# Performance work log

Measured on AMD Instinct MI355X. Metric: run time of the kernel, lower is better.

## Reference

```python
import jax, jax.numpy as jnp
import numpy as np

HEAD_NUM = 6

def setup_inputs() -> dict:
    key = jax.random.key(0)
    k1, k2, k3 = jax.random.split(key, 3)
    B, N, P, C = 4, 64, 256, 384
    x = jax.random.normal(k1, (B, N, P, C), dtype=jnp.float32)
    # torch Linear init scale ~ 1/sqrt(fan_in); keep magnitudes sane
    w_qkv = jax.random.normal(k2, (C, 3 * C), dtype=jnp.float32) * (1.0 / np.sqrt(C))
    w_proj = jax.random.normal(k3, (C, C), dtype=jnp.float32) * (1.0 / np.sqrt(C))
    b_proj = jnp.zeros((C,), dtype=jnp.float32)
    return {"x": x, "w_qkv": w_qkv, "w_proj": w_proj, "b_proj": b_proj}

def reference(x, w_qkv, w_proj, b_proj):
    B, N, P, C = x.shape
    H = HEAD_NUM
    D = C // H
    scale = jnp.asarray(D, dtype=x.dtype)  # NOTE: head_dim ** 1, faithful to source
    qkv = (x @ w_qkv).reshape(B, N, P, 3, H, D)
    q = qkv[:, :, :, 0]  # (B, N, P, H, D)
    k = qkv[:, :, :, 1]
    v = qkv[:, :, :, 2]
    attn = jnp.einsum('bnphd,bnqhd->bnhpq', q, k) * scale  # (B,N,H,P,P)
    attn = jax.nn.softmax(attn, axis=-1)
    out = jnp.einsum('bnhpq,bnqhd->bnphd', attn, v).reshape(B, N, P, C)
    return out @ w_proj + b_proj
```

## Files before the change

### kernel.cpp

```cpp
#include <hip/hip_runtime.h>

typedef __bf16 bf16_t;
typedef __bf16 bf16x8 __attribute__((ext_vector_type(8)));
typedef float f32x4 __attribute__((ext_vector_type(4)));
typedef unsigned short u16;
typedef unsigned short u16x4 __attribute__((ext_vector_type(4)));
typedef unsigned int u32;

#define B_ 4
#define N_ 64
#define P_ 256
#define C_ 384
#define H_ 6
#define D_ 64
#define M_TOTAL 65536
#define NQKV 1152
#define KSTEPS 12
#define NBLK (H_*B_*N_)
#define WKS_BYTES 24576
#define WKS_U16   12288
#define FUSED_LDS 139264
#define PB_STRIDE 40
#define SB() __builtin_amdgcn_sched_barrier(0)

#define GLOAD_LDS16(g, l) __builtin_amdgcn_global_load_lds( \
    (const __attribute__((address_space(1))) void*)(g), \
    (__attribute__((address_space(3))) void*)(l), 16, 0, 0)

__device__ __forceinline__ u16 f2b(float f){ return __builtin_bit_cast(u16, (bf16_t)f); }
__device__ __forceinline__ f32x4 mfma(bf16x8 a, bf16x8 b, f32x4 c){
    return __builtin_amdgcn_mfma_f32_16x16x32_bf16(a, b, c, 0, 0, 0);
}

__global__ __launch_bounds__(256) void prep_w(
    const float* __restrict__ wqkv, const float* __restrict__ wproj,
    u16* __restrict__ Wpk, u16* __restrict__ wPt)
{
    int i = blockIdx.x * 256 + threadIdx.x;
    const int NSLOT = H_ * KSTEPS * 12 * 64;
    if (i < NSLOT) {
        int lane = i & 63;
        int frag = i >> 6;
        int nf = frag % 12;
        int ks = (frag / 12) % KSTEPS;
        int h  = frag / (12 * KSTEPS);
        int part = nf >> 2;
        int nh   = (nf & 3) * 16 + (lane & 15);
        int col  = part * C_ + h * 64 + nh;
        int k0   = ks * 32 + (lane >> 4) * 8;
        size_t base = (size_t)(h * KSTEPS + ks) * WKS_U16 + nf * 512 + lane * 8;
        #pragma unroll
        for (int e = 0; e < 8; ++e) {
            float w = wqkv[(size_t)(k0 + e) * NQKV + col];
            bf16_t hi = (bf16_t)w;
            Wpk[base + e]        = __builtin_bit_cast(u16, hi);
            Wpk[base + 6144 + e] = f2b(w - (float)hi);
        }
    }
    int j = i - NSLOT;
    if (j >= 0 && j < C_ * C_) {
        int k = j / C_, n = j % C_;
        wPt[(size_t)n * C_ + k] = f2b(wproj[j]);
    }
}

__global__ __launch_bounds__(512, 2) void fused_attn(
    const float* __restrict__ x, const u16* __restrict__ Wpk,
    u16* __restrict__ attn)
{
    extern __shared__ u16 sm[];
    u16* Kh = sm;
    u16* Kl = sm + 16384;
    u16* Vt = sm + 32768;
    u16* Qb = sm + 49152;

    const int tid  = threadIdx.x;
    const int lane = tid & 63, wid = tid >> 6;
    const int g = lane >> 4, r16 = lane & 15;

    const int p = blockIdx.x;
    const int logical = (p & 7) * (NBLK / 8) + (p >> 3);
    const int h  = logical % H_;
    const int bn = logical / H_;
    const size_t row0 = (size_t)bn * P_;
    const int m0w = wid * 32;

    f32x4 acc[2][12];
    #pragma unroll
    for (int mf = 0; mf < 2; ++mf)
        #pragma unroll
        for (int nf = 0; nf < 12; ++nf) acc[mf][nf] = f32x4{0.f,0.f,0.f,0.f};

    const float* xr0 = x + (row0 + m0w + r16) * C_;
    const float* xr1 = xr0 + 16 * C_;
    const char* wbase = (const char*)Wpk + (size_t)h * (KSTEPS * WKS_BYTES);

#define STAGE(ks_, par_) do { \
    const char* _gp = wbase + (size_t)(ks_) * WKS_BYTES; \
    char* _lp = (char*)(sm + (par_) * WKS_U16); \
    GLOAD_LDS16(_gp + tid * 16,          _lp + tid * 16); \
    GLOAD_LDS16(_gp + 8192 + tid * 16,   _lp + 8192 + tid * 16); \
    GLOAD_LDS16(_gp + 16384 + tid * 16,  _lp + 16384 + tid * 16); \
} while (0)

    f32x4 xr[2][4];
#define XLOAD(ks_, par_) do { \
    const float* _xp0 = xr0 + (ks_) * 32 + 8 * g; \
    const float* _xp1 = xr1 + (ks_) * 32 + 8 * g; \
    xr[par_][0] = *(const f32x4*)_xp0; xr[par_][1] = *(const f32x4*)(_xp0 + 4); \
    xr[par_][2] = *(const f32x4*)_xp1; xr[par_][3] = *(const f32x4*)(_xp1 + 4); \
} while (0)

    bf16x8 ah[2], al[2];
#define SPLIT_A(par_) do { \
    _Pragma("unroll") \
    for (int e = 0; e < 4; ++e) { \
        bf16_t h0 = (bf16_t)xr[par_][0][e], h1 = (bf16_t)xr[par_][1][e]; \
        ah[0][e]   = h0; al[0][e]   = (bf16_t)(xr[par_][0][e] - (float)h0); \
        ah[0][4+e] = h1; al[0][4+e] = (bf16_t)(xr[par_][1][e] - (float)h1); \
        bf16_t h2 = (bf16_t)xr[par_][2][e], h3 = (bf16_t)xr[par_][3][e]; \
        ah[1][e]   = h2; al[1][e]   = (bf16_t)(xr[par_][2][e] - (float)h2); \
        ah[1][4+e] = h3; al[1][4+e] = (bf16_t)(xr[par_][3][e] - (float)h3); \
    } } while (0)

    STAGE(0, 0);
    XLOAD(0, 0);
    __syncthreads();

    #pragma unroll
    for (int ks = 0; ks < KSTEPS; ++ks) {
        const int par = ks & 1, nxt = par ^ 1;
        if (ks < KSTEPS - 1) {
            STAGE(ks + 1, nxt);
            XLOAD(ks + 1, nxt);
        }
        SPLIT_A(par);
        const u16* stg = sm + par * WKS_U16;
        #pragma unroll
        for (int nf = 0; nf < 8; ++nf) {
            bf16x8 bh = *(const bf16x8*)&stg[nf * 512 + lane * 8];
            bf16x8 bl = *(const bf16x8*)&stg[6144 + nf * 512 + lane * 8];
            acc[0][nf] = mfma(ah[0], bh, acc[0][nf]);
            acc[1][nf] = mfma(ah[1], bh, acc[1][nf]);
            acc[0][nf] = mfma(ah[0], bl, acc[0][nf]);
            acc[1][nf] = mfma(ah[1], bl, acc[1][nf]);
            acc[0][nf] = mfma(al[0], bh, acc[0][nf]);
            acc[1][nf] = mfma(al[1], bh, acc[1][nf]);
        }
        #pragma unroll
        for (int nf = 8; nf < 12; ++nf) {
            bf16x8 bh = *(const bf16x8*)&stg[nf * 512 + lane * 8];
            acc[0][nf] = mfma(ah[0], bh, acc[0][nf]);
            acc[1][nf] = mfma(ah[1], bh, acc[1][nf]);
        }
        __syncthreads();
    }

    #pragma unroll
    for (int mf = 0; mf < 2; ++mf)
    #pragma unroll
    for (int f = 0; f < 4; ++f)
    #pragma unroll
    for (int rr = 0; rr < 4; ++rr) {
        int q = m0w + mf * 16 + 4 * g + rr;
        int d = f * 16 + r16;
        int ek = q * 64 + (((d >> 3) ^ (q & 7)) << 3) + (d & 7);
        float kv = acc[mf][4 + f][rr];
        bf16_t khi = (bf16_t)kv;
        Kh[ek] = __builtin_bit_cast(u16, khi);
        Kl[ek] = f2b(kv - (float)khi);
        Vt[d * 256 + (((q >> 3) ^ (d & 7)) << 3) + (q & 7)] = f2b(acc[mf][8 + f][rr]);
    }

    u16* myQb = Qb + wid * 2560;
    bf16x8 aqh[2][2], aql[2][2];
    #pragma unroll
    for (int mf = 0; mf < 2; ++mf)
    #pragma unroll
    for (int f = 0; f < 4; ++f)
    #pragma unroll
    for (int rr = 0; rr < 4; ++rr) {
        int r = mf * 16 + 4 * g + rr;
        int c = f * 16 + r16;
        myQb[r * 64 + (((c >> 3) ^ (r & 7)) << 3) + (c & 7)] = f2b(acc[mf][f][rr]);
    }
    #pragma unroll
    for (int mf = 0; mf < 2; ++mf)
    #pragma unroll
    for (int k2 = 0; k2 < 2; ++k2) {
        int r = mf * 16 + r16;
        aqh[mf][k2] = *(const bf16x8*)&myQb[r * 64 + (((k2 * 4 + g) ^ (r & 7)) << 3)];
    }
    SB();
    #pragma unroll
    for (int mf = 0; mf < 2; ++mf)
    #pragma unroll
    for (int f = 0; f < 4; ++f)
    #pragma unroll
    for (int rr = 0; rr < 4; ++rr) {
        int r = mf * 16 + 4 * g + rr;
        int c = f * 16 + r16;
        float v = acc[mf][f][rr];
        bf16_t hi = (bf16_t)v;
        myQb[r * 64 + (((c >> 3) ^ (r & 7)) << 3) + (c & 7)] = f2b(v - (float)hi);
    }
    #pragma unroll
    for (int mf = 0; mf < 2; ++mf)
    #pragma unroll
    for (int k2 = 0; k2 < 2; ++k2) {
        int r = mf * 16 + r16;
        aql[mf][k2] = *(const bf16x8*)&myQb[r * 64 + (((k2 * 4 + g) ^ (r & 7)) << 3)];
    }

    __syncthreads();

    f32x4 S[2][16];
    #pragma unroll
    for (int mf = 0; mf < 2; ++mf)
        #pragma unroll
        for (int nf = 0; nf < 16; ++nf) S[mf][nf] = f32x4{0.f,0.f,0.f,0.f};

    bf16x8 khv[2][2], klv[2][2];
    {
        int q = r16;
        #pragma unroll
        for (int k2 = 0; k2 < 2; ++k2) {
            int e = q * 64 + (((k2 * 4 + g) ^ (q & 7)) << 3);
            khv[0][k2] = *(const bf16x8*)&Kh[e];
            klv[0][k2] = *(const bf16x8*)&Kl[e];
        }
    }
    #pragma unroll
    for (int nf = 0; nf < 16; ++nf) {
        const int par = nf & 1, nxt = par ^ 1;
        if (nf < 15) {
            int q = (nf + 1) * 16 + r16;
            #pragma unroll
            for (int k2 = 0; k2 < 2; ++k2) {
                int e = q * 64 + (((k2 * 4 + g) ^ (q & 7)) << 3);
                khv[nxt][k2] = *(const bf16x8*)&Kh[e];
                klv[nxt][k2] = *(const bf16x8*)&Kl[e];
            }
        }
        SB();
        __builtin_amdgcn_s_setprio(1);
        #pragma unroll
        for (int k2 = 0; k2 < 2; ++k2) {
            S[0][nf] = mfma(aqh[0][k2], khv[par][k2], S[0][nf]);
            S[1][nf] = mfma(aqh[1][k2], khv[par][k2], S[1][nf]);
            S[0][nf] = mfma(aqh[0][k2], klv[par][k2], S[0][nf]);
            S[1][nf] = mfma(aqh[1][k2], klv[par][k2], S[1][nf]);
            S[0][nf] = mfma(aql[0][k2], khv[par][k2], S[0][nf]);
            S[1][nf] = mfma(aql[1][k2], khv[par][k2], S[1][nf]);
        }
        __builtin_amdgcn_s_setprio(0);
        SB();
    }

    float inv_[2][4];
    #pragma unroll
    for (int mf = 0; mf < 2; ++mf) {
        float mrow[4] = {-1e30f,-1e30f,-1e30f,-1e30f};
        #pragma unroll
        for (int nf = 0; nf < 16; ++nf)
            #pragma unroll
            for (int rr = 0; rr < 4; ++rr) mrow[rr] = fmaxf(mrow[rr], S[mf][nf][rr]);
        #pragma unroll
        for (int mask = 1; mask < 16; mask <<= 1)
            #pragma unroll
            for (int rr = 0; rr < 4; ++rr) mrow[rr] = fmaxf(mrow[rr], __shfl_xor(mrow[rr], mask, 64));
        float ssum[4] = {0.f,0.f,0.f,0.f};
        #pragma unroll
        for (int nf = 0; nf < 16; ++nf)
            #pragma unroll
            for (int rr = 0; rr < 4; ++rr) {
                float pv = __expf((S[mf][nf][rr] - mrow[rr]) * 64.0f);
                S[mf][nf][rr] = pv;
                ssum[rr] += pv;
            }
        #pragma unroll
        for (int mask = 1; mask < 16; mask <<= 1)
            #pragma unroll
            for (int rr = 0; rr < 4; ++rr) ssum[rr] += __shfl_xor(ssum[rr], mask, 64);
        #pragma unroll
        for (int rr = 0; rr < 4; ++rr) inv_[mf][rr] = 1.0f / ssum[rr];
    }

    f32x4 O[2][4];
    #pragma unroll
    for (int mf = 0; mf < 2; ++mf)
        #pragma unroll
        for (int f = 0; f < 4; ++f) O[mf][f] = f32x4{0.f,0.f,0.f,0.f};

    bf16x8 bvv[2][4];
    #pragma unroll
    for (int f = 0; f < 4; ++f) {
        int d = f * 16 + r16;
        bvv[0][f] = *(const bf16x8*)&Vt[d * 256 + ((((8 * g) >> 3) ^ (d & 7)) << 3)];
    }
    #pragma unroll
    for (int t = 0; t < 8; ++t) {
        const int par = t & 1, nxt = par ^ 1;
        if (t < 7) {
            #pragma unroll
            for (int f = 0; f < 4; ++f) {
                int d = f * 16 + r16;
                bvv[nxt][f] = *(const bf16x8*)&Vt[d * 256 + (((((t + 1) * 32 + 8 * g) >> 3) ^ (d & 7)) << 3)];
            }
        }
        u16* pb = myQb + par * 1280;
        #pragma unroll
        for (int mf = 0; mf < 2; ++mf)
        #pragma unroll
        for (int tt = 0; tt < 2; ++tt) {
            int nf = 2 * t + tt;
            #pragma unroll
            for (int rr = 0; rr < 4; ++rr)
                pb[(mf * 16 + 4 * g + rr) * PB_STRIDE + tt * 16 + r16] = f2b(S[mf][nf][rr] * inv_[mf][rr]);
        }
        bf16x8 ap0 = *(const bf16x8*)&pb[(r16) * PB_STRIDE + 8 * g];
        bf16x8 ap1 = *(const bf16x8*)&pb[(16 + r16) * PB_STRIDE + 8 * g];
        __builtin_amdgcn_s_setprio(1);
        #pragma unroll
        for (int f = 0; f < 4; ++f) {
            O[0][f] = mfma(ap0, bvv[par][f], O[0][f]);
            O[1][f] = mfma(ap1, bvv[par][f], O[1][f]);
        }
        __builtin_amdgcn_s_setprio(0);
    }

    #pragma unroll
    for (int mf = 0; mf < 2; ++mf)
    #pragma unroll
    for (int f = 0; f < 4; ++f)
    #pragma unroll
    for (int rr = 0; rr < 4; ++rr)
        attn[(row0 + m0w + mf * 16 + 4 * g + rr) * C_ + h * 64 + f * 16 + r16] = f2b(O[mf][f][rr]);
}

__global__ __launch_bounds__(256, 2) void proj_kernel(
    const u16* __restrict__ attn, const u16* __restrict__ wPt,
    const float* __restrict__ bias, float* __restrict__ out)
{
    __shared__ alignas(16) u16 As[128*32];
    __shared__ alignas(16) u16 Bs[128*32];

    const int tid = threadIdx.x;
    const int lane = tid & 63, wid = tid >> 6;
    const int wr = wid >> 1, wc = wid & 1;
    const int g = lane >> 4, r16 = lane & 15;
    const int m0 = blockIdx.x * 128;
    const int n0 = blockIdx.y * 128;

    f32x4 acc[4][4];
    for (int i = 0; i < 4; i++) for (int j = 0; j < 4; j++) acc[i][j] = f32x4{0.f,0.f,0.f,0.f};

    for (int kt = 0; kt < C_; kt += 32) {
        for (int r = 0; r < 4; ++r) {
            int i = tid + 256*r;
            int mm = i >> 3;
            int kk = (i & 7) << 2;
            u16x4 v = *(const u16x4*)&attn[(size_t)(m0+mm)*C_ + kt + kk];
            int e = mm*32 + (((kk>>3) ^ ((mm>>1)&3))<<3) + (kk&7);
            *(u16x4*)&As[e] = v;
        }
        for (int r = 0; r < 4; ++r) {
            int i = tid + 256*r;
            int nn = i >> 3;
            int kk = (i & 7) << 2;
            u16x4 v = *(const u16x4*)&wPt[(size_t)(n0+nn)*C_ + kt + kk];
            int e = nn*32 + (((kk>>3) ^ ((nn>>1)&3))<<3) + (kk&7);
            *(u16x4*)&Bs[e] = v;
        }
        __syncthreads();

        bf16x8 a[4], b[4];
        for (int i = 0; i < 4; i++) {
            int row = wr*64 + i*16 + r16;
            a[i] = *(const bf16x8*)&As[row*32 + ((g ^ ((row>>1)&3))<<3)];
        }
        for (int j = 0; j < 4; j++) {
            int n = wc*64 + j*16 + r16;
            b[j] = *(const bf16x8*)&Bs[n*32 + ((g ^ ((n>>1)&3))<<3)];
        }
        for (int i = 0; i < 4; i++) for (int j = 0; j < 4; j++)
            acc[i][j] = mfma(a[i], b[j], acc[i][j]);
        __syncthreads();
    }

    for (int i = 0; i < 4; i++) for (int j = 0; j < 4; j++) for (int rr = 0; rr < 4; rr++) {
        size_t row = m0 + wr*64 + i*16 + g*4 + rr;
        int col = n0 + wc*64 + j*16 + r16;
        out[row*C_ + col] = acc[i][j][rr] + bias[col];
    }
}

extern "C" void kernel_launch(void* const* d_in, const int* in_sizes, int n_in,
                              void* d_out, int out_size, void* d_ws, size_t ws_size,
                              hipStream_t stream)
{
    const float* x      = (const float*)d_in[0];
    const float* w_qkv  = (const float*)d_in[1];
    const float* w_proj = (const float*)d_in[2];
    const float* b_proj = (const float*)d_in[3];
    float* out = (float*)d_out;

    u16* ws = (u16*)d_ws;
    u16* attnb = ws;
    size_t off = (size_t)M_TOTAL * C_;
    u16* Wpk = ws + off; off += (size_t)H_ * KSTEPS * WKS_U16;
    u16* wPt = ws + off; off += (size_t)C_ * C_;

    hipFuncSetAttribute((const void*)fused_attn,
                        hipFuncAttributeMaxDynamicSharedMemorySize, FUSED_LDS);

    int prep_n = H_ * KSTEPS * 12 * 64 + C_ * C_;
    prep_w<<<dim3((prep_n + 255) / 256), 256, 0, stream>>>(w_qkv, w_proj, Wpk, wPt);
    fused_attn<<<dim3(NBLK), 512, FUSED_LDS, stream>>>(x, Wpk, attnb);
    proj_kernel<<<dim3(M_TOTAL / 128, C_ / 128), 256, 0, stream>>>(attnb, wPt, b_proj, out);
}
```

Baseline: 265.6 us.

## Split fused attention across 16 waves with 16-row tiles and slimmer weight staging

The fused QKV+attention kernel goes from 512 to 1024 threads, so each wave handles 16 query rows instead of 32. This roughly halves the per-wave accumulator and score registers. The weight staging buffer drops the unused low-precision halves for the V slices, and the Q/P scratch space is moved into the freed staging region. The V-fragment double buffering is removed and softmax normalization is applied before packing P. The aim is more latency hiding from more resident waves. The risk is that the aggressive launch bound (1024, 4) forces a very tight register budget and spills, while the fixed LDS footprint still allows only one block per CU.

```diff
diff --git a/kernel.cpp b/kernel.cpp
--- a/kernel.cpp
+++ b/kernel.cpp
@@ -17,8 +17,8 @@
 #define NQKV 1152
 #define KSTEPS 12
 #define NBLK (H_*B_*N_)
-#define WKS_BYTES 24576
-#define WKS_U16   12288
+#define WKS_U16 10240
+#define WKS_BYTES 20480
 #define FUSED_LDS 139264
 #define PB_STRIDE 40
 #define SB() __builtin_amdgcn_sched_barrier(0)
@@ -48,13 +48,14 @@
         int nh   = (nf & 3) * 16 + (lane & 15);
         int col  = part * C_ + h * 64 + nh;
         int k0   = ks * 32 + (lane >> 4) * 8;
-        size_t base = (size_t)(h * KSTEPS + ks) * WKS_U16 + nf * 512 + lane * 8;
+        size_t base = (size_t)(h * KSTEPS + ks) * WKS_U16;
         #pragma unroll
         for (int e = 0; e < 8; ++e) {
             float w = wqkv[(size_t)(k0 + e) * NQKV + col];
             bf16_t hi = (bf16_t)w;
-            Wpk[base + e]        = __builtin_bit_cast(u16, hi);
-            Wpk[base + 6144 + e] = f2b(w - (float)hi);
+            Wpk[base + nf * 512 + lane * 8 + e] = __builtin_bit_cast(u16, hi);
+            if (nf < 8)
+                Wpk[base + 6144 + nf * 512 + lane * 8 + e] = f2b(w - (float)hi);
         }
     }
     int j = i - NSLOT;
@@ -64,7 +65,7 @@
     }
 }
 
-__global__ __launch_bounds__(512, 2) void fused_attn(
+__global__ __launch_bounds__(1024, 4) void fused_attn(
     const float* __restrict__ x, const u16* __restrict__ Wpk,
     u16* __restrict__ attn)
 {
@@ -72,7 +73,6 @@
     u16* Kh = sm;
     u16* Kl = sm + 16384;
     u16* Vt = sm + 32768;
-    u16* Qb = sm + 49152;
 
     const int tid  = threadIdx.x;
     const int lane = tid & 63, wid = tid >> 6;
@@ -83,44 +83,35 @@
     const int h  = logical % H_;
     const int bn = logical / H_;
     const size_t row0 = (size_t)bn * P_;
-    const int m0w = wid * 32;
-
-    f32x4 acc[2][12];
-    #pragma unroll
-    for (int mf = 0; mf < 2; ++mf)
-        #pragma unroll
-        for (int nf = 0; nf < 12; ++nf) acc[mf][nf] = f32x4{0.f,0.f,0.f,0.f};
+    const int m0w = wid * 16;
+
+    f32x4 acc[12];
+    #pragma unroll
+    for (int nf = 0; nf < 12; ++nf) acc[nf] = f32x4{0.f,0.f,0.f,0.f};
 
     const float* xr0 = x + (row0 + m0w + r16) * C_;
-    const float* xr1 = xr0 + 16 * C_;
     const char* wbase = (const char*)Wpk + (size_t)h * (KSTEPS * WKS_BYTES);
 
 #define STAGE(ks_, par_) do { \
     const char* _gp = wbase + (size_t)(ks_) * WKS_BYTES; \
-    char* _lp = (char*)(sm + (par_) * WKS_U16); \
-    GLOAD_LDS16(_gp + tid * 16,          _lp + tid * 16); \
-    GLOAD_LDS16(_gp + 8192 + tid * 16,   _lp + 8192 + tid * 16); \
-    GLOAD_LDS16(_gp + 16384 + tid * 16,  _lp + 16384 + tid * 16); \
+    char* _lp = (char*)(sm + 49152 + (par_) * WKS_U16); \
+    GLOAD_LDS16(_gp + tid * 16, _lp + tid * 16); \
+    if (tid < 256) GLOAD_LDS16(_gp + 16384 + tid * 16, _lp + 16384 + tid * 16); \
 } while (0)
 
-    f32x4 xr[2][4];
+    f32x4 xr[2][2];
 #define XLOAD(ks_, par_) do { \
-    const float* _xp0 = xr0 + (ks_) * 32 + 8 * g; \
-    const float* _xp1 = xr1 + (ks_) * 32 + 8 * g; \
-    xr[par_][0] = *(const f32x4*)_xp0; xr[par_][1] = *(const f32x4*)(_xp0 + 4); \
-    xr[par_][2] = *(const f32x4*)_xp1; xr[par_][3] = *(const f32x4*)(_xp1 + 4); \
+    const float* _xp = xr0 + (ks_) * 32 + 8 * g; \
+    xr[par_][0] = *(const f32x4*)_xp; xr[par_][1] = *(const f32x4*)(_xp + 4); \
 } while (0)
 
-    bf16x8 ah[2], al[2];
+    bf16x8 ah, al;
 #define SPLIT_A(par_) do { \
     _Pragma("unroll") \
     for (int e = 0; e < 4; ++e) { \
         bf16_t h0 = (bf16_t)xr[par_][0][e], h1 = (bf16_t)xr[par_][1][e]; \
-        ah[0][e]   = h0; al[0][e]   = (bf16_t)(xr[par_][0][e] - (float)h0); \
-        ah[0][4+e] = h1; al[0][4+e] = (bf16_t)(xr[par_][1][e] - (float)h1); \
-        bf16_t h2 = (bf16_t)xr[par_][2][e], h3 = (bf16_t)xr[par_][3][e]; \
-        ah[1][e]   = h2; al[1][e]   = (bf16_t)(xr[par_][2][e] - (float)h2); \
-        ah[1][4+e] = h3; al[1][4+e] = (bf16_t)(xr[par_][3][e] - (float)h3); \
+        ah[e]   = h0; al[e]   = (bf16_t)(xr[par_][0][e] - (float)h0); \
+        ah[4+e] = h1; al[4+e] = (bf16_t)(xr[par_][1][e] - (float)h1); \
     } } while (0)
 
     STAGE(0, 0);
@@ -135,90 +126,70 @@
             XLOAD(ks + 1, nxt);
         }
         SPLIT_A(par);
-        const u16* stg = sm + par * WKS_U16;
+        const u16* stg = sm + 49152 + par * WKS_U16;
         #pragma unroll
         for (int nf = 0; nf < 8; ++nf) {
             bf16x8 bh = *(const bf16x8*)&stg[nf * 512 + lane * 8];
             bf16x8 bl = *(const bf16x8*)&stg[6144 + nf * 512 + lane * 8];
-            acc[0][nf] = mfma(ah[0], bh, acc[0][nf]);
-            acc[1][nf] = mfma(ah[1], bh, acc[1][nf]);
-            acc[0][nf] = mfma(ah[0], bl, acc[0][nf]);
-            acc[1][nf] = mfma(ah[1], bl, acc[1][nf]);
-            acc[0][nf] = mfma(al[0], bh, acc[0][nf]);
-            acc[1][nf] = mfma(al[1], bh, acc[1][nf]);
+            acc[nf] = mfma(ah, bh, acc[nf]);
+            acc[nf] = mfma(ah, bl, acc[nf]);
+            acc[nf] = mfma(al, bh, acc[nf]);
         }
         #pragma unroll
         for (int nf = 8; nf < 12; ++nf) {
             bf16x8 bh = *(const bf16x8*)&stg[nf * 512 + lane * 8];
-            acc[0][nf] = mfma(ah[0], bh, acc[0][nf]);
-            acc[1][nf] = mfma(ah[1], bh, acc[1][nf]);
+            acc[nf] = mfma(ah, bh, acc[nf]);
         }
         __syncthreads();
     }
 
     #pragma unroll
-    for (int mf = 0; mf < 2; ++mf)
-    #pragma unroll
     for (int f = 0; f < 4; ++f)
     #pragma unroll
     for (int rr = 0; rr < 4; ++rr) {
-        int q = m0w + mf * 16 + 4 * g + rr;
+        int q = m0w + 4 * g + rr;
         int d = f * 16 + r16;
         int ek = q * 64 + (((d >> 3) ^ (q & 7)) << 3) + (d & 7);
-        float kv = acc[mf][4 + f][rr];
+        float kv = acc[4 + f][rr];
         bf16_t khi = (bf16_t)kv;
         Kh[ek] = __builtin_bit_cast(u16, khi);
         Kl[ek] = f2b(kv - (float)khi);
-        Vt[d * 256 + (((q >> 3) ^ (d & 7)) << 3) + (q & 7)] = f2b(acc[mf][8 + f][rr]);
-    }
-
-    u16* myQb = Qb + wid * 2560;
-    bf16x8 aqh[2][2], aql[2][2];
-    #pragma unroll
-    for (int mf = 0; mf < 2; ++mf)
+        Vt[d * 256 + (((q >> 3) ^ (d & 7)) << 3) + (q & 7)] = f2b(acc[8 + f][rr]);
+    }
+
+    u16* myQb = sm + 49152 + wid * 1024;
+    bf16x8 aqh[2], aql[2];
     #pragma unroll
     for (int f = 0; f < 4; ++f)
     #pragma unroll
     for (int rr = 0; rr < 4; ++rr) {
-        int r = mf * 16 + 4 * g + rr;
+        int r = 4 * g + rr;
         int c = f * 16 + r16;
-        myQb[r * 64 + (((c >> 3) ^ (r & 7)) << 3) + (c & 7)] = f2b(acc[mf][f][rr]);
-    }
-    #pragma unroll
-    for (int mf = 0; mf < 2; ++mf)
-    #pragma unroll
-    for (int k2 = 0; k2 < 2; ++k2) {
-        int r = mf * 16 + r16;
-        aqh[mf][k2] = *(const bf16x8*)&myQb[r * 64 + (((k2 * 4 + g) ^ (r & 7)) << 3)];
-    }
+        myQb[r * 64 + (((c >> 3) ^ (r & 7)) << 3) + (c & 7)] = f2b(acc[f][rr]);
+    }
+    #pragma unroll
+    for (int k2 = 0; k2 < 2; ++k2)
+        aqh[k2] = *(const bf16x8*)&myQb[r16 * 64 + (((k2 * 4 + g) ^ (r16 & 7)) << 3)];
     SB();
     #pragma unroll
-    for (int mf = 0; mf < 2; ++mf)
-    #pragma unroll
     for (int f = 0; f < 4; ++f)
     #pragma unroll
     for (int rr = 0; rr < 4; ++rr) {
-        int r = mf * 16 + 4 * g + rr;
+        int r = 4 * g + rr;
         int c = f * 16 + r16;
-        float v = acc[mf][f][rr];
+        float v = acc[f][rr];
         bf16_t hi = (bf16_t)v;
         myQb[r * 64 + (((c >> 3) ^ (r & 7)) << 3) + (c & 7)] = f2b(v - (float)hi);
     }
     #pragma unroll
-    for (int mf = 0; mf < 2; ++mf)
-    #pragma unroll
-    for (int k2 = 0; k2 < 2; ++k2) {
-        int r = mf * 16 + r16;
-        aql[mf][k2] = *(const bf16x8*)&myQb[r * 64 + (((k2 * 4 + g) ^ (r & 7)) << 3)];
-    }
+    for (int k2 = 0; k2 < 2; ++k2)
+        aql[k2] = *(const bf16x8*)&myQb[r16 * 64 + (((k2 * 4 + g) ^ (r16 & 7)) << 3)];
 
     __syncthreads();
 
-    f32x4 S[2][16];
-    #pragma unroll
-    for (int mf = 0; mf < 2; ++mf)
-        #pragma unroll
-        for (int nf = 0; nf < 16; ++nf) S[mf][nf] = f32x4{0.f,0.f,0.f,0.f};
+    f32x4 S[16];
+    #pragma unroll
+    for (int nf = 0; nf < 16; ++nf) S[nf] = f32x4{0.f,0.f,0.f,0.f};
 
     bf16x8 khv[2][2], klv[2][2];
     {
@@ -246,25 +217,20 @@
         __builtin_amdgcn_s_setprio(1);
         #pragma unroll
         for (int k2 = 0; k2 < 2; ++k2) {
-            S[0][nf] = mfma(aqh[0][k2], khv[par][k2], S[0][nf]);
-            S[1][nf] = mfma(aqh[1][k2], khv[par][k2], S[1][nf]);
-            S[0][nf] = mfma(aqh[0][k2], klv[par][k2], S[0][nf]);
-            S[1][nf] = mfma(aqh[1][k2], klv[par][k2], S[1][nf]);
-            S[0][nf] = mfma(aql[0][k2], khv[par][k2], S[0][nf]);
-            S[1][nf] = mfma(aql[1][k2], khv[par][k2], S[1][nf]);
+            S[nf] = mfma(aqh[k2], khv[par][k2], S[nf]);
+            S[nf] = mfma(aqh[k2], klv[par][k2], S[nf]);
+            S[nf] = mfma(aql[k2], khv[par][k2], S[nf]);
         }
         __builtin_amdgcn_s_setprio(0);
         SB();
     }
 
-    float inv_[2][4];
-    #pragma unroll
-    for (int mf = 0; mf < 2; ++mf) {
+    {
         float mrow[4] = {-1e30f,-1e30f,-1e30f,-1e30f};
         #pragma unroll
         for (int nf = 0; nf < 16; ++nf)
             #pragma unroll
-            for (int rr = 0; rr < 4; ++rr) mrow[rr] = fmaxf(mrow[rr], S[mf][nf][rr]);
+            for (int rr = 0; rr < 4; ++rr) mrow[rr] = fmaxf(mrow[rr], S[nf][rr]);
         #pragma unroll
         for (int mask = 1; mask < 16; mask <<= 1)
             #pragma unroll
@@ -274,68 +240,55 @@
         for (int nf = 0; nf < 16; ++nf)
             #pragma unroll
             for (int rr = 0; rr < 4; ++rr) {
-                float pv = __expf((S[mf][nf][rr] - mrow[rr]) * 64.0f);
-                S[mf][nf][rr] = pv;
+                float pv = __expf((S[nf][rr] - mrow[rr]) * 64.0f);
+                S[nf][rr] = pv;
                 ssum[rr] += pv;
             }
         #pragma unroll
         for (int mask = 1; mask < 16; mask <<= 1)
             #pragma unroll
             for (int rr = 0; rr < 4; ++rr) ssum[rr] += __shfl_xor(ssum[rr], mask, 64);
-        #pragma unroll
-        for (int rr = 0; rr < 4; ++rr) inv_[mf][rr] = 1.0f / ssum[rr];
-    }
-
-    f32x4 O[2][4];
-    #pragma unroll
-    for (int mf = 0; mf < 2; ++mf)
-        #pragma unroll
-        for (int f = 0; f < 4; ++f) O[mf][f] = f32x4{0.f,0.f,0.f,0.f};
-
-    bf16x8 bvv[2][4];
-    #pragma unroll
-    for (int f = 0; f < 4; ++f) {
-        int d = f * 16 + r16;
-        bvv[0][f] = *(const bf16x8*)&Vt[d * 256 + ((((8 * g) >> 3) ^ (d & 7)) << 3)];
-    }
+        float inv_[4];
+        #pragma unroll
+        for (int rr = 0; rr < 4; ++rr) inv_[rr] = 1.0f / ssum[rr];
+        #pragma unroll
+        for (int nf = 0; nf < 16; ++nf)
+            #pragma unroll
+            for (int rr = 0; rr < 4; ++rr) S[nf][rr] *= inv_[rr];
+    }
+
+    f32x4 O[4];
+    #pragma unroll
+    for (int f = 0; f < 4; ++f) O[f] = f32x4{0.f,0.f,0.f,0.f};
+
+    u16* pb = sm + 49152 + wid * 640;
     #pragma unroll
     for (int t = 0; t < 8; ++t) {
-        const int par = t & 1, nxt = par ^ 1;
-        if (t < 7) {
-            #pragma unroll
-            for (int f = 0; f < 4; ++f) {
-                int d = f * 16 + r16;
-                bvv[nxt][f] = *(const bf16x8*)&Vt[d * 256 + (((((t + 1) * 32 + 8 * g) >> 3) ^ (d & 7)) << 3)];
-            }
-        }
-        u16* pb = myQb + par * 1280;
-        #pragma unroll
-        for (int mf = 0; mf < 2; ++mf)
+        bf16x8 bv[4];
+        #pragma unroll
+        for (int f = 0; f < 4; ++f) {
+            int d = f * 16 + r16;
+            bv[f] = *(const bf16x8*)&Vt[d * 256 + ((((t * 32 + 8 * g) >> 3) ^ (d & 7)) << 3)];
+        }
         #pragma unroll
         for (int tt = 0; tt < 2; ++tt) {
             int nf = 2 * t + tt;
             #pragma unroll
             for (int rr = 0; rr < 4; ++rr)
-                pb[(mf * 16 + 4 * g + rr) * PB_STRIDE + tt * 16 + r16] = f2b(S[mf][nf][rr] * inv_[mf][rr]);
-        }
-        bf16x8 ap0 = *(const bf16x8*)&pb[(r16) * PB_STRIDE + 8 * g];
-        bf16x8 ap1 = *(const bf16x8*)&pb[(16 + r16) * PB_STRIDE + 8 * g];
+                pb[(4 * g + rr) * PB_STRIDE + tt * 16 + r16] = f2b(S[nf][rr]);
+        }
+        bf16x8 ap = *(const bf16x8*)&pb[r16 * PB_STRIDE + 8 * g];
         __builtin_amdgcn_s_setprio(1);
         #pragma unroll
-        for (int f = 0; f < 4; ++f) {
-            O[0][f] = mfma(ap0, bvv[par][f], O[0][f]);
-            O[1][f] = mfma(ap1, bvv[par][f], O[1][f]);
-        }
+        for (int f = 0; f < 4; ++f) O[f] = mfma(ap, bv[f], O[f]);
         __builtin_amdgcn_s_setprio(0);
     }
 
     #pragma unroll
-    for (int mf = 0; mf < 2; ++mf)
-    #pragma unroll
     for (int f = 0; f < 4; ++f)
     #pragma unroll
     for (int rr = 0; rr < 4; ++rr)
-        attn[(row0 + m0w + mf * 16 + 4 * g + rr) * C_ + h * 64 + f * 16 + r16] = f2b(O[mf][f][rr]);
+        attn[(row0 + m0w + 4 * g + rr) * C_ + h * 64 + f * 16 + r16] = f2b(O[f][rr]);
 }
 
 __global__ __launch_bounds__(256, 2) void proj_kernel(
@@ -416,6 +369,6 @@
 
     int prep_n = H_ * KSTEPS * 12 * 64 + C_ * C_;
     prep_w<<<dim3((prep_n + 255) / 256), 256, 0, stream>>>(w_qkv, w_proj, Wpk, wPt);
-    fused_attn<<<dim3(NBLK), 512, FUSED_LDS, stream>>>(x, Wpk, attnb);
+    fused_attn<<<dim3(NBLK), 1024, FUSED_LDS, stream>>>(x, Wpk, attnb);
     proj_kernel<<<dim3(M_TOTAL / 128, C_ / 128), 256, 0, stream>>>(attnb, wPt, b_proj, out);
 }
```

Result: faster. 248.6 us (-6.4%).
